# Performance work log

Hardware: AMD Instinct MI355X
Metric: run time of the kernel (lower is better)

## Reference

```python
import jax, jax.numpy as jnp
import numpy as np

C = 256
CI = C // 2  # inter_channels


def conv1x1(x, w, b):
    # x: [B,C,H,W], w: [O,C], b: [O] -> [B,O,H,W]
    return jnp.einsum('bchw,oc->bohw', x, w) + b[None, :, None, None]


def setup_inputs() -> dict:
    key = jax.random.key(0)
    ks = jax.random.split(key, 9)
    B, H, W = 8, 56, 56
    s = 0.02
    return {
        'x': jax.random.normal(ks[0], (B, C, H, W), dtype=jnp.float32),
        'g_w': jax.random.normal(ks[1], (CI, C), dtype=jnp.float32) * s,
        'g_b': jax.random.normal(ks[2], (CI,), dtype=jnp.float32) * s,
        'theta_w': jax.random.normal(ks[3], (CI, C), dtype=jnp.float32) * s,
        'theta_b': jax.random.normal(ks[4], (CI,), dtype=jnp.float32) * s,
        'phi_w': jax.random.normal(ks[5], (CI, C), dtype=jnp.float32) * s,
        'phi_b': jax.random.normal(ks[6], (CI,), dtype=jnp.float32) * s,
        'W_w': jax.random.normal(ks[7], (C, CI), dtype=jnp.float32) * s,
        'W_b': jax.random.normal(ks[8], (C,), dtype=jnp.float32) * s,
    }


def reference(x, g_w, g_b, theta_w, theta_b, phi_w, phi_b, W_w, W_b):
    B, Cc, H, Wd = x.shape
    N = H * Wd
    g_x = conv1x1(x, g_w, g_b).reshape(B, CI, N).transpose(0, 2, 1)        # [B,N,CI]
    theta_x = conv1x1(x, theta_w, theta_b).reshape(B, CI, N).transpose(0, 2, 1)  # [B,N,CI]
    phi_x = conv1x1(x, phi_w, phi_b).reshape(B, CI, N)                     # [B,CI,N]
    f = jnp.einsum('bnc,bcm->bnm', theta_x, phi_x)                         # [B,N,N]
    attn = jax.nn.softmax(f, axis=-1)
    y = jnp.einsum('bnm,bmc->bnc', attn, g_x)                              # [B,N,CI]
    y = y.transpose(0, 2, 1).reshape(B, CI, H, Wd)                         # [B,CI,H,W]
    z = conv1x1(y, W_w, W_b) + x
    return z
```

## Files before the change

kernel.cpp:

```cpp
#include <hip/hip_runtime.h>

#define NB 8
#define C 256
#define CI 128
#define NPIX 3136
#define NT 64
#define NTILES 49
#define NGQ 13
#define NROWT 98
#define NSPLIT 4
#define LOG2E 1.44269504f

typedef unsigned short u16;
typedef unsigned int u32;
typedef __bf16 bf16x8 __attribute__((ext_vector_type(8)));
typedef float f32x4 __attribute__((ext_vector_type(4)));
typedef float f32x16 __attribute__((ext_vector_type(16)));

static __device__ __forceinline__ u16 f2b(float f) {
  union { float f; u32 u; } v; v.f = f;
  u32 r = v.u + 0x7FFFu + ((v.u >> 16) & 1u);
  return (u16)(r >> 16);
}
static __device__ __forceinline__ float b2f(u16 v) {
  union { u32 u; float f; } x; x.u = ((u32)v) << 16; return x.f;
}
static __device__ __forceinline__ u32 cvtpk(float lo, float hi) {
  u32 r;
  asm("v_cvt_pk_bf16_f32 %0, %1, %2" : "=v"(r) : "v"(lo), "v"(hi));
  return r;
}
static __device__ __forceinline__ void swap32(u32& x, u32& y) {
  asm("v_permlane32_swap_b32 %0, %1" : "+v"(x), "+v"(y));
}
static __device__ __forceinline__ void gl16(const void* g, void* l) {
  __builtin_amdgcn_global_load_lds(
      (const __attribute__((address_space(1))) u32*)g,
      (__attribute__((address_space(3))) u32*)l, 16, 0, 0);
}

__global__ __launch_bounds__(256) void k0_convert(
    const float* __restrict__ g_w, const float* __restrict__ th_w,
    const float* __restrict__ ph_w, const float* __restrict__ W_w,
    u16* __restrict__ wcat, u16* __restrict__ Wbf) {
  int i = blockIdx.x * 256 + threadIdx.x;
  if (i < 98304) {
    int o = i >> 8, c = i & 255;
    float v = (o < 128) ? g_w[o * 256 + c]
            : (o < 256) ? th_w[(o - 128) * 256 + c] * LOG2E
                        : ph_w[(o - 256) * 256 + c];
    wcat[i] = f2b(v);
  } else {
    int j = i - 98304;
    Wbf[j] = f2b(W_w[j]);
  }
}

__global__ __launch_bounds__(256) void k1_proj(
    const float* __restrict__ x, const float* __restrict__ g_b,
    const float* __restrict__ th_b, const float* __restrict__ ph_b,
    const u16* __restrict__ wcat, u16* __restrict__ thO,
    u16* __restrict__ phO, u16* __restrict__ gO) {
  __shared__ __align__(16) u16 xT[32 * 264];
  char* xTb = reinterpret_cast<char*>(xT);
  int tid = threadIdx.x;
  int b = blockIdx.x / NROWT, nt = blockIdx.x % NROWT;
  int n0 = nt * 32;
  const float* xb = x + (size_t)b * C * NPIX;
  {
    int c0 = tid >> 3, nq = tid & 7;
    for (int k = 0; k < 8; ++k) {
      int c = c0 + 32 * k;
      float4 xv = *reinterpret_cast<const float4*>(xb + (size_t)c * NPIX + n0 + 4 * nq);
      float vals[4] = {xv.x, xv.y, xv.z, xv.w};
#pragma unroll
      for (int j = 0; j < 4; ++j) {
        int row = 4 * nq + j;
        xT[row * 264 + c] = f2b(vals[j]);
      }
    }
  }
  __syncthreads();
  int wave = tid >> 6, lane = tid & 63;
  int wq = wave & 1, wo = wave >> 1;
  int r = 16 * wq + (lane & 15);
  bf16x8 a[8];
#pragma unroll
  for (int kk = 0; kk < 8; ++kk) {
    int ch = 4 * kk + (lane >> 4);
    a[kk] = *reinterpret_cast<const bf16x8*>(xTb + r * 528 + ch * 16);
  }
  for (int os = 12 * wo; os < 12 * wo + 12; ++os) {
    int o = 16 * os + (lane & 15);
    f32x4 acc = {0.f, 0.f, 0.f, 0.f};
    const u16* wrow = wcat + (size_t)o * 256 + 8 * (lane >> 4);
#pragma unroll
    for (int kk = 0; kk < 8; ++kk) {
      bf16x8 bb = *reinterpret_cast<const bf16x8*>(wrow + 32 * kk);
      acc = __builtin_amdgcn_mfma_f32_16x16x32_bf16(a[kk], bb, acc, 0, 0, 0);
    }
    int p = os >> 3;
    int ol = (os & 7) * 16 + (lane & 15);
    const float* bias = (p == 0) ? g_b : (p == 1) ? th_b : ph_b;
    float bv = bias[ol];
    if (p == 1) bv *= LOG2E;
    int nbase = n0 + 16 * wq + 4 * (lane >> 4);
    if (p == 0) {
      ushort4 pk;
      pk.x = f2b(acc[0] + bv); pk.y = f2b(acc[1] + bv);
      pk.z = f2b(acc[2] + bv); pk.w = f2b(acc[3] + bv);
      *reinterpret_cast<ushort4*>(gO + ((size_t)b * CI + ol) * NPIX + nbase) = pk;
    } else {
      u16* dst = (p == 1) ? thO : phO;
#pragma unroll
      for (int j = 0; j < 4; ++j)
        dst[((size_t)b * NPIX + nbase + j) * CI + ol] = f2b(acc[j] + bv);
    }
  }
}

__global__ __launch_bounds__(512, 2) void k2_attn(
    const u16* __restrict__ th, const u16* __restrict__ ph,
    const u16* __restrict__ gbuf, u16* __restrict__ yp,
    float* __restrict__ lm) {
  __shared__ __align__(16) char lds[65536];
  int tid = threadIdx.x, wave = tid >> 6, lane = tid & 63;
  int h5 = lane >> 5, l31 = lane & 31;
  int bid = blockIdx.x;
  int s = bid & 3, rest = bid >> 2;
  int b = rest / NGQ, ng = rest % NGQ;
  int qbase = ng * 256 + wave * 32;
  if (qbase + 32 > NPIX) qbase = NPIX - 32;
  int ts = (NTILES * s) >> 2, te = (NTILES * (s + 1)) >> 2;

  bf16x8 bth[8];
  {
    const u16* trow = th + ((size_t)b * NPIX + qbase + l31) * CI;
#pragma unroll
    for (int ks = 0; ks < 8; ++ks)
      bth[ks] = *reinterpret_cast<const bf16x8*>(trow + 16 * ks + 8 * h5);
  }
  float lrun = 0.f;
  f32x16 zv;
#pragma unroll
  for (int j = 0; j < 16; ++j) zv[j] = 0.f;
  f32x16 yacc[4];
#pragma unroll
  for (int cb = 0; cb < 4; ++cb)
#pragma unroll
    for (int j = 0; j < 16; ++j) yacc[cb][j] = 0.f;

  auto stage = [&](int buf, int mt) {
    int m0 = mt * NT;
    char* phB = lds + buf * 16384;
    char* gB = lds + 32768 + buf * 16384;
#pragma unroll
    for (int c = 0; c < 2; ++c) {
      int call = wave * 2 + c;
      int o = call * 1024 + lane * 16;
      int row = o >> 8, chl = (o >> 4) & 15;
      int chg = chl ^ (row & 15);
      gl16(ph + ((size_t)(b * NPIX + m0 + row)) * CI + chg * 8, phB + call * 1024);
    }
#pragma unroll
    for (int c = 0; c < 2; ++c) {
      int call = wave * 2 + c;
      int o = call * 1024 + lane * 16;
      int ci = o >> 7, chl = (o >> 4) & 7;
      int chg = chl ^ (ci & 7);
      gl16(gbuf + ((size_t)b * CI + ci) * NPIX + m0 + chg * 8, gB + call * 1024);
    }
  };

  stage(0, ts);
  int cur = 0;
  for (int mt = ts; mt < te; ++mt) {
    bool pre = (mt + 1 < te);
    if (pre) stage(cur ^ 1, mt + 1);
    if (pre) {
      asm volatile("s_waitcnt vmcnt(4)" ::: "memory");
    } else {
      asm volatile("s_waitcnt vmcnt(0)" ::: "memory");
    }
    __builtin_amdgcn_s_barrier();
    __builtin_amdgcn_sched_barrier(0);
    char* phB = lds + cur * 16384;
    char* gB = lds + 32768 + cur * 16384;
    f32x16 sv0, sv1;
    __builtin_amdgcn_s_setprio(1);
    {
      int off = l31 * 256 + ((h5 ^ (l31 & 15)) << 4);
      bf16x8 a0 = *reinterpret_cast<const bf16x8*>(phB + off);
      bf16x8 a1 = *reinterpret_cast<const bf16x8*>(phB + off + 8192);
      sv0 = __builtin_amdgcn_mfma_f32_32x32x16_bf16(a0, bth[0], zv, 0, 0, 0);
      sv1 = __builtin_amdgcn_mfma_f32_32x32x16_bf16(a1, bth[0], zv, 0, 0, 0);
    }
#pragma unroll
    for (int ks = 1; ks < 8; ++ks) {
      int chk = 2 * ks + h5;
      int off = l31 * 256 + ((chk ^ (l31 & 15)) << 4);
      bf16x8 a0 = *reinterpret_cast<const bf16x8*>(phB + off);
      bf16x8 a1 = *reinterpret_cast<const bf16x8*>(phB + off + 8192);
      sv0 = __builtin_amdgcn_mfma_f32_32x32x16_bf16(a0, bth[ks], sv0, 0, 0, 0);
      sv1 = __builtin_amdgcn_mfma_f32_32x32x16_bf16(a1, bth[ks], sv1, 0, 0, 0);
    }
    __builtin_amdgcn_s_setprio(0);
#pragma unroll
    for (int j = 0; j < 16; ++j) {
      sv0[j] = exp2f(sv0[j]);
      sv1[j] = exp2f(sv1[j]);
    }
    float a0 = 0.f, a1 = 0.f, a2 = 0.f, a3 = 0.f;
#pragma unroll
    for (int i = 0; i < 16; i += 4) {
      a0 += sv0[i] + sv1[i];
      a1 += sv0[i + 1] + sv1[i + 1];
      a2 += sv0[i + 2] + sv1[i + 2];
      a3 += sv0[i + 3] + sv1[i + 3];
    }
    lrun += (a0 + a1) + (a2 + a3);
    u32 pk[2][4][2];
#pragma unroll
    for (int t = 0; t < 4; ++t) {
      pk[0][t][0] = cvtpk(sv0[4 * t], sv0[4 * t + 1]);
      pk[0][t][1] = cvtpk(sv0[4 * t + 2], sv0[4 * t + 3]);
      pk[1][t][0] = cvtpk(sv1[4 * t], sv1[4 * t + 1]);
      pk[1][t][1] = cvtpk(sv1[4 * t + 2], sv1[4 * t + 3]);
    }
    __builtin_amdgcn_s_setprio(1);
#pragma unroll
    for (int ks = 0; ks < 4; ++ks) {
      int m2 = ks >> 1, t0 = 2 * (ks & 1);
      swap32(pk[m2][t0][0], pk[m2][t0 + 1][0]);
      swap32(pk[m2][t0][1], pk[m2][t0 + 1][1]);
      union { u32 u[4]; bf16x8 v; } f;
      f.u[0] = pk[m2][t0][0]; f.u[1] = pk[m2][t0][1];
      f.u[2] = pk[m2][t0 + 1][0]; f.u[3] = pk[m2][t0 + 1][1];
      int chk = 2 * ks + h5;
#pragma unroll
      for (int cb = 0; cb < 4; ++cb) {
        int ci = 32 * cb + l31;
        bf16x8 gv = *reinterpret_cast<const bf16x8*>(
            gB + ci * 128 + ((chk ^ (ci & 7)) << 4));
        yacc[cb] = __builtin_amdgcn_mfma_f32_32x32x16_bf16(f.v, gv, yacc[cb], 0, 0, 0);
      }
    }
    __builtin_amdgcn_s_setprio(0);
    __builtin_amdgcn_sched_barrier(0);
    asm volatile("s_waitcnt lgkmcnt(0)" ::: "memory");
    __builtin_amdgcn_s_barrier();
    cur ^= 1;
  }
  lrun += __shfl_xor(lrun, 32);
  u16* ypb = yp + (size_t)(s * NB + b) * NPIX * CI;
#pragma unroll
  for (int cb = 0; cb < 4; ++cb)
#pragma unroll
    for (int j = 0; j < 16; ++j) {
      int n = qbase + (j & 3) + 8 * (j >> 2) + 4 * h5;
      ypb[(size_t)n * CI + 32 * cb + l31] = f2b(yacc[cb][j]);
    }
  if (lane < 32) {
    int n = qbase + l31;
    lm[(size_t)(s * NB + b) * NPIX + n] = lrun;
  }
}

__global__ __launch_bounds__(256) void k3_out(
    const u16* __restrict__ yp, const float* __restrict__ lm,
    const u16* __restrict__ Wbf, const float* __restrict__ W_b,
    const float* __restrict__ x, float* __restrict__ z) {
  __shared__ __align__(16) u16 yT[32 * 136];
  int tid = threadIdx.x, wave = tid >> 6, lane = tid & 63;
  int b = blockIdx.x / NROWT, nt = blockIdx.x % NROWT;
  int n0 = nt * 32;
#pragma unroll
  for (int i = 0; i < 2; ++i) {
    int qq = tid + i * 256;
    int row = qq >> 4, ch = qq & 15;
    int n = n0 + row;
    float den = 0.f;
    float num[8];
#pragma unroll
    for (int e = 0; e < 8; ++e) num[e] = 0.f;
#pragma unroll
    for (int s = 0; s < NSPLIT; ++s) {
      den += lm[(size_t)(s * NB + b) * NPIX + n];
      union { uint4 u4; u16 us[8]; } yv;
      yv.u4 = *reinterpret_cast<const uint4*>(
          yp + (size_t)(s * NB + b) * NPIX * CI + (size_t)n * CI + ch * 8);
#pragma unroll
      for (int e = 0; e < 8; ++e) num[e] += b2f(yv.us[e]);
    }
    float inv = 1.f / den;
    union { uint4 u4; u16 us[8]; } ov;
#pragma unroll
    for (int e = 0; e < 8; ++e) ov.us[e] = f2b(num[e] * inv);
    *reinterpret_cast<uint4*>(yT + row * 136 + ch * 8) = ov.u4;
  }
  __syncthreads();
  int q = lane >> 4, l15 = lane & 15;
  int wq = wave & 1, wo = wave >> 1;
  int n = n0 + 16 * wq + l15;
  bf16x8 bf[4];
#pragma unroll
  for (int kk = 0; kk < 4; ++kk)
    bf[kk] = *reinterpret_cast<const bf16x8*>(yT + (16 * wq + l15) * 136 + 32 * kk + 8 * q);
  for (int os = 8 * wo; os < 8 * wo + 8; ++os) {
    f32x4 acc = {0.f, 0.f, 0.f, 0.f};
    const u16* wrow = Wbf + (size_t)(16 * os + l15) * 128 + 8 * q;
#pragma unroll
    for (int kk = 0; kk < 4; ++kk) {
      bf16x8 aw = *reinterpret_cast<const bf16x8*>(wrow + 32 * kk);
      acc = __builtin_amdgcn_mfma_f32_16x16x32_bf16(aw, bf[kk], acc, 0, 0, 0);
    }
    float4 bwv = *reinterpret_cast<const float4*>(W_b + 16 * os + 4 * q);
    float bw[4] = {bwv.x, bwv.y, bwv.z, bwv.w};
#pragma unroll
    for (int j = 0; j < 4; ++j) {
      size_t off = ((size_t)b * C + 16 * os + 4 * q + j) * NPIX + n;
      z[off] = acc[j] + bw[j] + x[off];
    }
  }
}

extern "C" void kernel_launch(void* const* d_in, const int* in_sizes, int n_in,
                              void* d_out, int out_size, void* d_ws, size_t ws_size,
                              hipStream_t stream) {
  const float* x    = (const float*)d_in[0];
  const float* g_w  = (const float*)d_in[1];
  const float* g_b  = (const float*)d_in[2];
  const float* th_w = (const float*)d_in[3];
  const float* th_b = (const float*)d_in[4];
  const float* ph_w = (const float*)d_in[5];
  const float* ph_b = (const float*)d_in[6];
  const float* W_w  = (const float*)d_in[7];
  const float* W_b  = (const float*)d_in[8];
  float* z = (float*)d_out;
  u16* ws = (u16*)d_ws;
  u16* wcat = ws;
  u16* Wbf  = ws + 98304;
  u16* th   = ws + 131072;
  u16* phb  = th + 3211264;
  u16* gbb  = phb + 3211264;
  u16* yp   = gbb + 3211264;
  float* lm = (float*)(ws + 131072 + (size_t)3211264 * 7);
  hipLaunchKernelGGL(k0_convert, dim3(512), dim3(256), 0, stream,
                     g_w, th_w, ph_w, W_w, wcat, Wbf);
  hipLaunchKernelGGL(k1_proj, dim3(NB * NROWT), dim3(256), 0, stream,
                     x, g_b, th_b, ph_b, wcat, th, phb, gbb);
  hipLaunchKernelGGL(k2_attn, dim3(NB * NGQ * NSPLIT), dim3(512), 0, stream,
                     th, phb, gbb, yp, lm);
  hipLaunchKernelGGL(k3_out, dim3(NB * NROWT), dim3(256), 0, stream,
                     yp, lm, Wbf, W_b, x, z);
}
```

Baseline: 152.6 us.

## Fuse split-K reduction and output projection into attention via last-block counter

Removes the weight-conversion kernel by converting fp32 weights to bf16 on the fly inside the projection kernels. Fuses the output conv into the attention kernel: each of the four split blocks increments an atomic counter, and the last one to finish reduces the partial results with cache-bypassing loads and computes the residual output. This drops two kernel launches and their tails, at the cost of atomics, fences and serialized tail work done only by the last-arriving blocks.

```diff
diff --git a/kernel.cpp b/kernel.cpp
--- a/kernel.cpp
+++ b/kernel.cpp
@@ -38,32 +38,47 @@
       (const __attribute__((address_space(1))) u32*)g,
       (__attribute__((address_space(3))) u32*)l, 16, 0, 0);
 }
-
-__global__ __launch_bounds__(256) void k0_convert(
-    const float* __restrict__ g_w, const float* __restrict__ th_w,
-    const float* __restrict__ ph_w, const float* __restrict__ W_w,
-    u16* __restrict__ wcat, u16* __restrict__ Wbf) {
-  int i = blockIdx.x * 256 + threadIdx.x;
-  if (i < 98304) {
-    int o = i >> 8, c = i & 255;
-    float v = (o < 128) ? g_w[o * 256 + c]
-            : (o < 256) ? th_w[(o - 128) * 256 + c] * LOG2E
-                        : ph_w[(o - 256) * 256 + c];
-    wcat[i] = f2b(v);
-  } else {
-    int j = i - 98304;
-    Wbf[j] = f2b(W_w[j]);
-  }
+static __device__ __forceinline__ void stsc_u16(void* p, u32 v) {
+  asm volatile("global_store_short %0, %1, off sc0 sc1" :: "v"(p), "v"(v) : "memory");
+}
+static __device__ __forceinline__ void stsc_f32(void* p, float v) {
+  asm volatile("global_store_dword %0, %1, off sc0 sc1" :: "v"(p), "v"(v) : "memory");
+}
+static __device__ __forceinline__ void ldsc4_u128(
+    const void* p0, const void* p1, const void* p2, const void* p3,
+    uint4& r0, uint4& r1, uint4& r2, uint4& r3) {
+  asm volatile(
+      "global_load_dwordx4 %0, %4, off sc0 sc1\n"
+      "global_load_dwordx4 %1, %5, off sc0 sc1\n"
+      "global_load_dwordx4 %2, %6, off sc0 sc1\n"
+      "global_load_dwordx4 %3, %7, off sc0 sc1\n"
+      "s_waitcnt vmcnt(0)"
+      : "=&v"(r0), "=&v"(r1), "=&v"(r2), "=&v"(r3)
+      : "v"(p0), "v"(p1), "v"(p2), "v"(p3) : "memory");
+}
+static __device__ __forceinline__ void ldsc4_f32(
+    const float* p0, const float* p1, const float* p2, const float* p3,
+    float& f0, float& f1, float& f2, float& f3) {
+  asm volatile(
+      "global_load_dword %0, %4, off sc0 sc1\n"
+      "global_load_dword %1, %5, off sc0 sc1\n"
+      "global_load_dword %2, %6, off sc0 sc1\n"
+      "global_load_dword %3, %7, off sc0 sc1\n"
+      "s_waitcnt vmcnt(0)"
+      : "=&v"(f0), "=&v"(f1), "=&v"(f2), "=&v"(f3)
+      : "v"(p0), "v"(p1), "v"(p2), "v"(p3) : "memory");
 }
 
 __global__ __launch_bounds__(256) void k1_proj(
     const float* __restrict__ x, const float* __restrict__ g_b,
     const float* __restrict__ th_b, const float* __restrict__ ph_b,
-    const u16* __restrict__ wcat, u16* __restrict__ thO,
-    u16* __restrict__ phO, u16* __restrict__ gO) {
+    const float* __restrict__ g_w, const float* __restrict__ th_w,
+    const float* __restrict__ ph_w, u16* __restrict__ thO,
+    u16* __restrict__ phO, u16* __restrict__ gO, u32* __restrict__ rc) {
   __shared__ __align__(16) u16 xT[32 * 264];
   char* xTb = reinterpret_cast<char*>(xT);
   int tid = threadIdx.x;
+  if (blockIdx.x < NB * NGQ && tid == 0) rc[blockIdx.x] = 0;
   int b = blockIdx.x / NROWT, nt = blockIdx.x % NROWT;
   int n0 = nt * 32;
   const float* xb = x + (size_t)b * C * NPIX;
@@ -74,37 +89,38 @@
       float4 xv = *reinterpret_cast<const float4*>(xb + (size_t)c * NPIX + n0 + 4 * nq);
       float vals[4] = {xv.x, xv.y, xv.z, xv.w};
 #pragma unroll
-      for (int j = 0; j < 4; ++j) {
-        int row = 4 * nq + j;
-        xT[row * 264 + c] = f2b(vals[j]);
-      }
+      for (int j = 0; j < 4; ++j)
+        xT[(4 * nq + j) * 264 + c] = f2b(vals[j]);
     }
   }
   __syncthreads();
   int wave = tid >> 6, lane = tid & 63;
+  int q = lane >> 4, l15 = lane & 15;
   int wq = wave & 1, wo = wave >> 1;
-  int r = 16 * wq + (lane & 15);
+  int r = 16 * wq + l15;
   bf16x8 a[8];
 #pragma unroll
-  for (int kk = 0; kk < 8; ++kk) {
-    int ch = 4 * kk + (lane >> 4);
-    a[kk] = *reinterpret_cast<const bf16x8*>(xTb + r * 528 + ch * 16);
-  }
+  for (int kk = 0; kk < 8; ++kk)
+    a[kk] = *reinterpret_cast<const bf16x8*>(xTb + r * 528 + (4 * kk + q) * 16);
   for (int os = 12 * wo; os < 12 * wo + 12; ++os) {
-    int o = 16 * os + (lane & 15);
+    int p = os >> 3;
+    int ol = (os & 7) * 16 + l15;
+    const float* wr = ((p == 0) ? g_w : (p == 1) ? th_w : ph_w) + (size_t)ol * 256 + 8 * q;
+    float sc = (p == 1) ? LOG2E : 1.f;
     f32x4 acc = {0.f, 0.f, 0.f, 0.f};
-    const u16* wrow = wcat + (size_t)o * 256 + 8 * (lane >> 4);
 #pragma unroll
     for (int kk = 0; kk < 8; ++kk) {
-      bf16x8 bb = *reinterpret_cast<const bf16x8*>(wrow + 32 * kk);
-      acc = __builtin_amdgcn_mfma_f32_16x16x32_bf16(a[kk], bb, acc, 0, 0, 0);
-    }
-    int p = os >> 3;
-    int ol = (os & 7) * 16 + (lane & 15);
+      float4 w0 = *reinterpret_cast<const float4*>(wr + 32 * kk);
+      float4 w1 = *reinterpret_cast<const float4*>(wr + 32 * kk + 4);
+      union { u32 u[4]; bf16x8 v8; } wb;
+      wb.u[0] = cvtpk(w0.x * sc, w0.y * sc); wb.u[1] = cvtpk(w0.z * sc, w0.w * sc);
+      wb.u[2] = cvtpk(w1.x * sc, w1.y * sc); wb.u[3] = cvtpk(w1.z * sc, w1.w * sc);
+      acc = __builtin_amdgcn_mfma_f32_16x16x32_bf16(a[kk], wb.v8, acc, 0, 0, 0);
+    }
     const float* bias = (p == 0) ? g_b : (p == 1) ? th_b : ph_b;
     float bv = bias[ol];
     if (p == 1) bv *= LOG2E;
-    int nbase = n0 + 16 * wq + 4 * (lane >> 4);
+    int nbase = n0 + 16 * wq + 4 * q;
     if (p == 0) {
       ushort4 pk;
       pk.x = f2b(acc[0] + bv); pk.y = f2b(acc[1] + bv);
@@ -119,10 +135,12 @@
   }
 }
 
-__global__ __launch_bounds__(512, 2) void k2_attn(
+__global__ __launch_bounds__(512, 2) void k2k3(
     const u16* __restrict__ th, const u16* __restrict__ ph,
     const u16* __restrict__ gbuf, u16* __restrict__ yp,
-    float* __restrict__ lm) {
+    float* __restrict__ lm, u32* __restrict__ rc,
+    const float* __restrict__ W_w, const float* __restrict__ W_b,
+    const float* __restrict__ x, float* __restrict__ z) {
   __shared__ __align__(16) char lds[65536];
   int tid = threadIdx.x, wave = tid >> 6, lane = tid & 63;
   int h5 = lane >> 5, l31 = lane & 31;
@@ -258,68 +276,82 @@
 #pragma unroll
     for (int j = 0; j < 16; ++j) {
       int n = qbase + (j & 3) + 8 * (j >> 2) + 4 * h5;
-      ypb[(size_t)n * CI + 32 * cb + l31] = f2b(yacc[cb][j]);
-    }
-  if (lane < 32) {
-    int n = qbase + l31;
-    lm[(size_t)(s * NB + b) * NPIX + n] = lrun;
-  }
-}
-
-__global__ __launch_bounds__(256) void k3_out(
-    const u16* __restrict__ yp, const float* __restrict__ lm,
-    const u16* __restrict__ Wbf, const float* __restrict__ W_b,
-    const float* __restrict__ x, float* __restrict__ z) {
-  __shared__ __align__(16) u16 yT[32 * 136];
-  int tid = threadIdx.x, wave = tid >> 6, lane = tid & 63;
-  int b = blockIdx.x / NROWT, nt = blockIdx.x % NROWT;
-  int n0 = nt * 32;
-#pragma unroll
-  for (int i = 0; i < 2; ++i) {
-    int qq = tid + i * 256;
-    int row = qq >> 4, ch = qq & 15;
-    int n = n0 + row;
-    float den = 0.f;
-    float num[8];
-#pragma unroll
-    for (int e = 0; e < 8; ++e) num[e] = 0.f;
-#pragma unroll
-    for (int s = 0; s < NSPLIT; ++s) {
-      den += lm[(size_t)(s * NB + b) * NPIX + n];
-      union { uint4 u4; u16 us[8]; } yv;
-      yv.u4 = *reinterpret_cast<const uint4*>(
-          yp + (size_t)(s * NB + b) * NPIX * CI + (size_t)n * CI + ch * 8);
-#pragma unroll
-      for (int e = 0; e < 8; ++e) num[e] += b2f(yv.us[e]);
-    }
-    float inv = 1.f / den;
-    union { uint4 u4; u16 us[8]; } ov;
-#pragma unroll
-    for (int e = 0; e < 8; ++e) ov.us[e] = f2b(num[e] * inv);
-    *reinterpret_cast<uint4*>(yT + row * 136 + ch * 8) = ov.u4;
-  }
+      stsc_u16(ypb + (size_t)n * CI + 32 * cb + l31, f2b(yacc[cb][j]));
+    }
+  if (lane < 32)
+    stsc_f32(lm + (size_t)(s * NB + b) * NPIX + qbase + l31, lrun);
+
+  __threadfence();
   __syncthreads();
-  int q = lane >> 4, l15 = lane & 15;
-  int wq = wave & 1, wo = wave >> 1;
-  int n = n0 + 16 * wq + l15;
-  bf16x8 bf[4];
-#pragma unroll
-  for (int kk = 0; kk < 4; ++kk)
-    bf[kk] = *reinterpret_cast<const bf16x8*>(yT + (16 * wq + l15) * 136 + 32 * kk + 8 * q);
-  for (int os = 8 * wo; os < 8 * wo + 8; ++os) {
-    f32x4 acc = {0.f, 0.f, 0.f, 0.f};
-    const u16* wrow = Wbf + (size_t)(16 * os + l15) * 128 + 8 * q;
-#pragma unroll
-    for (int kk = 0; kk < 4; ++kk) {
-      bf16x8 aw = *reinterpret_cast<const bf16x8*>(wrow + 32 * kk);
-      acc = __builtin_amdgcn_mfma_f32_16x16x32_bf16(aw, bf[kk], acc, 0, 0, 0);
-    }
-    float4 bwv = *reinterpret_cast<const float4*>(W_b + 16 * os + 4 * q);
-    float bw[4] = {bwv.x, bwv.y, bwv.z, bwv.w};
-#pragma unroll
-    for (int j = 0; j < 4; ++j) {
-      size_t off = ((size_t)b * C + 16 * os + 4 * q + j) * NPIX + n;
-      z[off] = acc[j] + bw[j] + x[off];
+  if (tid == 0)
+    *(volatile u32*)lds = (atomicAdd(&rc[rest], 1u) == 3u) ? 1u : 0u;
+  __syncthreads();
+  if (*(volatile u32*)lds == 0u) return;
+  __threadfence();
+
+  int half = tid >> 8, t2 = tid & 255;
+  u16* myT = reinterpret_cast<u16*>(lds + half * 16384);
+  for (int rep = 0; rep < 4; ++rep) {
+    __syncthreads();
+    int nt = ng * 8 + half + 2 * rep;
+    bool ok = nt < NROWT;
+    int n0 = nt * 32;
+    if (ok) {
+#pragma unroll
+      for (int i = 0; i < 2; ++i) {
+        int qq = t2 + i * 256;
+        int row = qq >> 4, ch = qq & 15;
+        int n = n0 + row;
+        uint4 y0, y1, y2, y3;
+        ldsc4_u128(yp + ((size_t)(0 * NB + b) * NPIX + n) * CI + ch * 8,
+                   yp + ((size_t)(1 * NB + b) * NPIX + n) * CI + ch * 8,
+                   yp + ((size_t)(2 * NB + b) * NPIX + n) * CI + ch * 8,
+                   yp + ((size_t)(3 * NB + b) * NPIX + n) * CI + ch * 8,
+                   y0, y1, y2, y3);
+        float l0, l1, l2, l3;
+        ldsc4_f32(lm + (size_t)(0 * NB + b) * NPIX + n,
+                  lm + (size_t)(1 * NB + b) * NPIX + n,
+                  lm + (size_t)(2 * NB + b) * NPIX + n,
+                  lm + (size_t)(3 * NB + b) * NPIX + n, l0, l1, l2, l3);
+        float inv = 1.f / (l0 + l1 + l2 + l3);
+        union { uint4 u4; u16 us[8]; } a4, b4, c4, d4, ov;
+        a4.u4 = y0; b4.u4 = y1; c4.u4 = y2; d4.u4 = y3;
+#pragma unroll
+        for (int e = 0; e < 8; ++e)
+          ov.us[e] = f2b((b2f(a4.us[e]) + b2f(b4.us[e]) + b2f(c4.us[e]) + b2f(d4.us[e])) * inv);
+        *reinterpret_cast<uint4*>(myT + row * 136 + ch * 8) = ov.u4;
+      }
+    }
+    __syncthreads();
+    if (ok) {
+      int w2 = t2 >> 6, ln = t2 & 63;
+      int q = ln >> 4, l15 = ln & 15;
+      int wq = w2 & 1, wo = w2 >> 1;
+      int n = n0 + 16 * wq + l15;
+      bf16x8 bf[4];
+#pragma unroll
+      for (int kk = 0; kk < 4; ++kk)
+        bf[kk] = *reinterpret_cast<const bf16x8*>(myT + (16 * wq + l15) * 136 + 32 * kk + 8 * q);
+      for (int os = 8 * wo; os < 8 * wo + 8; ++os) {
+        f32x4 acc = {0.f, 0.f, 0.f, 0.f};
+        const float* wr = W_w + (size_t)(16 * os + l15) * 128 + 8 * q;
+#pragma unroll
+        for (int kk = 0; kk < 4; ++kk) {
+          float4 w0 = *reinterpret_cast<const float4*>(wr + 32 * kk);
+          float4 w1 = *reinterpret_cast<const float4*>(wr + 32 * kk + 4);
+          union { u32 u[4]; bf16x8 v8; } wb;
+          wb.u[0] = cvtpk(w0.x, w0.y); wb.u[1] = cvtpk(w0.z, w0.w);
+          wb.u[2] = cvtpk(w1.x, w1.y); wb.u[3] = cvtpk(w1.z, w1.w);
+          acc = __builtin_amdgcn_mfma_f32_16x16x32_bf16(wb.v8, bf[kk], acc, 0, 0, 0);
+        }
+        float4 bwv = *reinterpret_cast<const float4*>(W_b + 16 * os + 4 * q);
+        float bw[4] = {bwv.x, bwv.y, bwv.z, bwv.w};
+#pragma unroll
+        for (int j = 0; j < 4; ++j) {
+          size_t off = ((size_t)b * C + 16 * os + 4 * q + j) * NPIX + n;
+          z[off] = acc[j] + bw[j] + x[off];
+        }
+      }
     }
   }
 }
@@ -338,19 +370,14 @@
   const float* W_b  = (const float*)d_in[8];
   float* z = (float*)d_out;
   u16* ws = (u16*)d_ws;
-  u16* wcat = ws;
-  u16* Wbf  = ws + 98304;
-  u16* th   = ws + 131072;
-  u16* phb  = th + 3211264;
-  u16* gbb  = phb + 3211264;
-  u16* yp   = gbb + 3211264;
-  float* lm = (float*)(ws + 131072 + (size_t)3211264 * 7);
-  hipLaunchKernelGGL(k0_convert, dim3(512), dim3(256), 0, stream,
-                     g_w, th_w, ph_w, W_w, wcat, Wbf);
+  u16* th  = ws;
+  u16* phb = th + 3211264;
+  u16* gbb = phb + 3211264;
+  u16* yp  = gbb + 3211264;
+  float* lm = (float*)(ws + (size_t)3211264 * 7);
+  u32* rc = (u32*)(lm + (size_t)NSPLIT * NB * NPIX);
   hipLaunchKernelGGL(k1_proj, dim3(NB * NROWT), dim3(256), 0, stream,
-                     x, g_b, th_b, ph_b, wcat, th, phb, gbb);
-  hipLaunchKernelGGL(k2_attn, dim3(NB * NGQ * NSPLIT), dim3(512), 0, stream,
-                     th, phb, gbb, yp, lm);
-  hipLaunchKernelGGL(k3_out, dim3(NB * NROWT), dim3(256), 0, stream,
-                     yp, lm, Wbf, W_b, x, z);
-}
+                     x, g_b, th_b, ph_b, g_w, th_w, ph_w, th, phb, gbb, rc);
+  hipLaunchKernelGGL(k2k3, dim3(NB * NGQ * NSPLIT), dim3(512), 0, stream,
+                     th, phb, gbb, yp, lm, rc, W_w, W_b, x, z);
+}
```

Result: slower. 419.0 us (+174.6%).
